# Kernel tuning notes

Measured on AMD Instinct MI355X. Metric: run time of the kernel, lower is better.

Reference implementation:

```python
import jax, jax.numpy as jnp
import numpy as np

B, S, D = 2, 2048, 2048
H = 16
HD = D // H  # 128
THETA = 10000.0


def setup_inputs() -> dict:
    key = jax.random.key(0)
    ks = jax.random.split(key, 5)
    return {
        "hidden_states": jax.random.normal(ks[0], (B, S, D), dtype=jnp.float32),
        "Wq": jax.random.normal(ks[1], (D, D), dtype=jnp.float32) * 0.02,
        "Wk": jax.random.normal(ks[2], (D, D), dtype=jnp.float32) * 0.02,
        "Wv": jax.random.normal(ks[3], (D, D), dtype=jnp.float32) * 0.02,
        "Wo": jax.random.normal(ks[4], (D, D), dtype=jnp.float32) * 0.02,
    }


def _rotate_half(x):
    x1, x2 = x[..., : HD // 2], x[..., HD // 2:]
    return jnp.concatenate([-x2, x1], axis=-1)


def _rope_cos_sin(seq_len, dtype):
    # freqs = 1/theta^(2i/d), i in [0, d/2)
    inv_freq = 1.0 / (THETA ** (jnp.arange(0, HD, 2, dtype=jnp.float32) / HD))
    ang = jnp.arange(seq_len, dtype=jnp.float32)[:, None] * inv_freq[None, :]  # [S, HD/2]
    cos = jnp.cos(ang).astype(dtype)
    sin = jnp.sin(ang).astype(dtype)
    # torch code does cos.repeat(1,1,1,2): tile halves -> [S, HD]
    cos2 = jnp.concatenate([cos, cos], axis=-1)[None, None]  # [1,1,S,HD]
    sin2 = jnp.concatenate([sin, sin], axis=-1)[None, None]
    return cos2, sin2


def reference(hidden_states, Wq, Wk, Wv, Wo):
    b, s, d = hidden_states.shape
    scale = 1.0 / np.sqrt(HD)
    # torch Linear: y = x @ W.T
    def proj(W):
        y = jnp.einsum("bsd,ed->bse", hidden_states, W)
        return y.reshape(b, s, H, HD).transpose(0, 2, 1, 3)  # [b,h,s,hd]
    q, k, v = proj(Wq), proj(Wk), proj(Wv)

    cos, sin = _rope_cos_sin(s, q.dtype)
    q = q * cos + _rotate_half(q) * sin
    k = k * cos + _rotate_half(k) * sin

    scores = jnp.einsum("bhqd,bhkd->bhqk", q, k) * scale
    # causal mask: -inf strictly above diagonal (kv_len == seq_len here)
    causal = jnp.triu(jnp.full((s, s), -jnp.inf, dtype=scores.dtype), k=1)
    scores = scores + causal[None, None]

    attn = jax.nn.softmax(scores.astype(jnp.float32), axis=-1).astype(q.dtype)
    ctx = jnp.einsum("bhqk,bhkd->bhqd", attn, v)
    ctx = ctx.transpose(0, 2, 1, 3).reshape(b, s, d)
    return jnp.einsum("bsd,ed->bse", ctx, Wo)
```

## Files before the change

### kernel.cpp

```cpp
#include <hip/hip_runtime.h>

typedef unsigned short ushort_t;
typedef __bf16 bf16x8 __attribute__((ext_vector_type(8)));
typedef float f32x4 __attribute__((ext_vector_type(4)));

#define S_LEN 2048
#define DMODEL 2048
#define NH 16
#define HDIM 128
#define BATCH 2
#define M_ROWS (BATCH * S_LEN)

__device__ __forceinline__ ushort_t f2bf(float f) {
    union { float f; unsigned u; } v; v.f = f;
    unsigned r = (v.u + 0x7fffu + ((v.u >> 16) & 1u)) >> 16;
    return (ushort_t)r;
}
__device__ __forceinline__ float bf2f(ushort_t u) {
    union { unsigned u; float f; } v; v.u = ((unsigned)u) << 16;
    return v.f;
}

__device__ __forceinline__ void async16(const void* g, void* l) {
    __builtin_amdgcn_global_load_lds(
        (const __attribute__((address_space(1))) void*)g,
        (__attribute__((address_space(3))) void*)l, 16, 0, 0);
}

__global__ void cvt_bf16(const float* __restrict__ in, ushort_t* __restrict__ out, int n4) {
    int i = blockIdx.x * blockDim.x + threadIdx.x;
    if (i >= n4) return;
    float4 f = ((const float4*)in)[i];
    ushort4 u;
    u.x = f2bf(f.x); u.y = f2bf(f.y); u.z = f2bf(f.z); u.w = f2bf(f.w);
    ((ushort4*)out)[i] = u;
}

__global__ void rope_tables(float* __restrict__ cosT, float* __restrict__ sinT) {
    int i = blockIdx.x * blockDim.x + threadIdx.x;
    int s = i >> 6, f = i & 63;
    float inv = powf(10000.0f, -(float)(2 * f) / 128.0f);
    float ang = (float)s * inv;
    cosT[i] = cosf(ang);
    sinT[i] = sinf(ang);
}

__global__ void rope_inplace(ushort_t* __restrict__ Q, ushort_t* __restrict__ K,
                             const float* __restrict__ cosT, const float* __restrict__ sinT) {
    long i = (long)blockIdx.x * blockDim.x + threadIdx.x;
    int f = (int)(i & 63);
    long t = i >> 6;
    int s = (int)(t & (S_LEN - 1));
    int bh = (int)(t >> 11);
    long base = ((long)bh * S_LEN + s) * HDIM;
    float c = cosT[s * 64 + f], sn = sinT[s * 64 + f];
    float a0 = bf2f(Q[base + f]), a1 = bf2f(Q[base + 64 + f]);
    Q[base + f]      = f2bf(a0 * c - a1 * sn);
    Q[base + 64 + f] = f2bf(a1 * c + a0 * sn);
    float b0 = bf2f(K[base + f]), b1 = bf2f(K[base + 64 + f]);
    K[base + f]      = f2bf(b0 * c - b1 * sn);
    K[base + 64 + f] = f2bf(b1 * c + b0 * sn);
}

template <int EPI>
__global__ __launch_bounds__(512) void gemm8(
    const ushort_t* __restrict__ A, const ushort_t* __restrict__ Bm,
    void* __restrict__ C0, void* __restrict__ C1, void* __restrict__ C2,
    int NB, int K) {
    __shared__ __align__(16) ushort_t As[2][128 * 64];
    __shared__ __align__(16) ushort_t Bs[2][256 * 64];
    const int tid = threadIdx.x;
    const int lane = tid & 63;
    const int w = tid >> 6;
    const int wm = w >> 2, wn = w & 3;
    const int fr = lane & 15, g = lane >> 4;
    const int nwg = gridDim.x;
    const int work = (blockIdx.x & 7) * (nwg >> 3) + (blockIdx.x >> 3);
    const int brow = (work / NB) * 128;
    const int bcol = (work % NB) * 256;

    int aRow[2], aK[2], bRow[4], bK[4];
#pragma unroll
    for (int q = 0; q < 2; q++) {
        int d = (q * 512 + tid) * 16;
        int s = d ^ (((d >> 9) & 1) << 5);
        aRow[q] = s >> 7; aK[q] = (s & 127) >> 1;
    }
#pragma unroll
    for (int q = 0; q < 4; q++) {
        int d = (q * 512 + tid) * 16;
        int s = d ^ (((d >> 9) & 1) << 5);
        bRow[q] = s >> 7; bK[q] = (s & 127) >> 1;
    }

    f32x4 acc[4][4];
#pragma unroll
    for (int m = 0; m < 4; m++)
#pragma unroll
        for (int n = 0; n < 4; n++) acc[m][n] = (f32x4){0.f, 0.f, 0.f, 0.f};

    auto stage = [&](int buf, int k0) {
#pragma unroll
        for (int q = 0; q < 2; q++)
            async16(&A[(long)(brow + aRow[q]) * K + k0 + aK[q]], &As[buf][(q * 512 + tid) * 8]);
#pragma unroll
        for (int q = 0; q < 4; q++)
            async16(&Bm[(long)(bcol + bRow[q]) * K + k0 + bK[q]], &Bs[buf][(q * 512 + tid) * 8]);
    };
    auto rdA = [&](int buf, int m, int ks) -> bf16x8 {
        int row = wm * 64 + m * 16 + fr;
        int off = row * 64 + ((ks * 32 + g * 8) ^ (((row >> 2) & 1) << 4));
        return *(const bf16x8*)&As[buf][off];
    };
    auto rdB = [&](int buf, int n, int ks) -> bf16x8 {
        int row = wn * 64 + n * 16 + fr;
        int off = row * 64 + ((ks * 32 + g * 8) ^ (((row >> 2) & 1) << 4));
        return *(const bf16x8*)&Bs[buf][off];
    };

    stage(0, 0);
    __syncthreads();

    const int NT = K / 64;
    int cur = 0;
    for (int kt = 0; kt < NT; ++kt) {
        if (kt + 1 < NT) stage(cur ^ 1, (kt + 1) * 64);
        bf16x8 a0[2][2], a2[2][2], bn[4][2];
#pragma unroll
        for (int m = 0; m < 2; m++)
#pragma unroll
            for (int ks = 0; ks < 2; ks++) a0[m][ks] = rdA(cur, m, ks);
#pragma unroll
        for (int n = 0; n < 2; n++)
#pragma unroll
            for (int ks = 0; ks < 2; ks++) bn[n][ks] = rdB(cur, n, ks);
        __builtin_amdgcn_s_setprio(1);
#pragma unroll
        for (int m = 0; m < 2; m++)
#pragma unroll
            for (int n = 0; n < 2; n++)
#pragma unroll
                for (int ks = 0; ks < 2; ks++)
                    acc[m][n] = __builtin_amdgcn_mfma_f32_16x16x32_bf16(a0[m][ks], bn[n][ks], acc[m][n], 0, 0, 0);
        __builtin_amdgcn_s_setprio(0);
#pragma unroll
        for (int n = 2; n < 4; n++)
#pragma unroll
            for (int ks = 0; ks < 2; ks++) bn[n][ks] = rdB(cur, n, ks);
        __builtin_amdgcn_s_setprio(1);
#pragma unroll
        for (int m = 0; m < 2; m++)
#pragma unroll
            for (int n = 2; n < 4; n++)
#pragma unroll
                for (int ks = 0; ks < 2; ks++)
                    acc[m][n] = __builtin_amdgcn_mfma_f32_16x16x32_bf16(a0[m][ks], bn[n][ks], acc[m][n], 0, 0, 0);
        __builtin_amdgcn_s_setprio(0);
#pragma unroll
        for (int m = 0; m < 2; m++)
#pragma unroll
            for (int ks = 0; ks < 2; ks++) a2[m][ks] = rdA(cur, m + 2, ks);
        __builtin_amdgcn_s_setprio(1);
#pragma unroll
        for (int m = 0; m < 2; m++)
#pragma unroll
            for (int n = 2; n < 4; n++)
#pragma unroll
                for (int ks = 0; ks < 2; ks++)
                    acc[m + 2][n] = __builtin_amdgcn_mfma_f32_16x16x32_bf16(a2[m][ks], bn[n][ks], acc[m + 2][n], 0, 0, 0);
        __builtin_amdgcn_s_setprio(0);
        __builtin_amdgcn_s_setprio(1);
#pragma unroll
        for (int m = 0; m < 2; m++)
#pragma unroll
            for (int n = 0; n < 2; n++)
#pragma unroll
                for (int ks = 0; ks < 2; ks++)
                    acc[m + 2][n] = __builtin_amdgcn_mfma_f32_16x16x32_bf16(a2[m][ks], bn[n][ks], acc[m + 2][n], 0, 0, 0);
        __builtin_amdgcn_s_setprio(0);
        __syncthreads();
        cur ^= 1;
    }

    const int rbase = brow + wm * 64;
    if constexpr (EPI == 0) {
        const int proj = bcol >> 11;
        const int cbase = (bcol & 2047) + wn * 64;
        if (proj < 2) {
            ushort_t* dst = (ushort_t*)(proj == 0 ? C0 : C1);
#pragma unroll
            for (int m = 0; m < 4; m++)
#pragma unroll
                for (int n = 0; n < 4; n++) {
                    int c2 = cbase + n * 16 + fr;
                    int h = c2 >> 7, hd = c2 & 127;
#pragma unroll
                    for (int r = 0; r < 4; r++) {
                        int row = rbase + m * 16 + g * 4 + r;
                        int b = row >> 11, s = row & (S_LEN - 1);
                        dst[(((long)(b * NH + h) * S_LEN) + s) * HDIM + hd] = f2bf(acc[m][n][r]);
                    }
                }
        } else {
            ushort_t* dst = (ushort_t*)C2;
#pragma unroll
            for (int m = 0; m < 4; m++) {
                int row0 = rbase + m * 16 + g * 4;
                int b = row0 >> 11, s0 = row0 & (S_LEN - 1);
#pragma unroll
                for (int n = 0; n < 4; n++) {
                    int c2 = cbase + n * 16 + fr;
                    int h = c2 >> 7, hd = c2 & 127;
                    ushort4 u;
                    u.x = f2bf(acc[m][n][0]); u.y = f2bf(acc[m][n][1]);
                    u.z = f2bf(acc[m][n][2]); u.w = f2bf(acc[m][n][3]);
                    *(ushort4*)&dst[(((long)(b * NH + h) * HDIM) + hd) * S_LEN + s0] = u;
                }
            }
        }
    } else {
        float* dst = (float*)C0;
#pragma unroll
        for (int m = 0; m < 4; m++)
#pragma unroll
            for (int n = 0; n < 4; n++) {
                int col = bcol + wn * 64 + n * 16 + fr;
#pragma unroll
                for (int r = 0; r < 4; r++) {
                    int row = rbase + m * 16 + g * 4 + r;
                    dst[(long)row * DMODEL + col] = acc[m][n][r];
                }
            }
    }
}

__global__ __launch_bounds__(256) void attn_fwd_v4(
    const ushort_t* __restrict__ Q, const ushort_t* __restrict__ K,
    const ushort_t* __restrict__ Vt, ushort_t* __restrict__ ctx) {
    __shared__ __align__(16) ushort_t Ks[2][64 * 128];
    __shared__ __align__(16) ushort_t Vs[2][128 * 64];
    __shared__ __align__(16) ushort_t Pls[4][16 * 64];

    const int tid = threadIdx.x;
    const int lane = tid & 63;
    const int w = tid >> 6;
    const int g = lane >> 4;
    const int fr = lane & 15;
    const int fk = g * 8;

    const int bid = blockIdx.x;
    const int xcd = bid & 7;
    const int t6 = bid >> 3;
    const int bh = xcd + 8 * (t6 & 3);
    const int p = t6 >> 2;
    const int qtA = p, qtB = 31 - p;
    const int b = bh >> 4, h = bh & 15;

    const ushort_t* Qb = Q + (long)bh * S_LEN * HDIM;
    const ushort_t* Kb = K + (long)bh * S_LEN * HDIM;
    const ushort_t* Vb = Vt + (long)bh * HDIM * S_LEN;

    int koff[4], voff[4], kdst[4], vdst[4];
#pragma unroll
    for (int r = 0; r < 4; r++) {
        int ci = r * 256 + tid;
        int krow = ci >> 4, kwc = ci & 15;
        koff[r] = krow * HDIM + ((kwc ^ (krow & 7)) * 8);
        kdst[r] = ci * 8;
        int vrow = ci >> 3, vwc = ci & 7;
        voff[r] = vrow * S_LEN + ((vwc ^ (vrow & 7)) * 8);
        vdst[r] = ci * 8;
    }
    auto stage = [&](int buf, int kv0) {
        const ushort_t* Kg = Kb + (long)kv0 * HDIM;
        const ushort_t* Vg = Vb + kv0;
#pragma unroll
        for (int r = 0; r < 4; r++) async16(Kg + koff[r], &Ks[buf][kdst[r]]);
#pragma unroll
        for (int r = 0; r < 4; r++) async16(Vg + voff[r], &Vs[buf][vdst[r]]);
    };

    int qrow0 = qtA * 64 + w * 16;
    bf16x8 qf[4];
    auto loadQ = [&]() {
#pragma unroll
        for (int t = 0; t < 4; t++)
            qf[t] = *(const bf16x8*)&Qb[(long)(qrow0 + fr) * HDIM + t * 32 + fk];
    };
    loadQ();

    f32x4 o[8];
#pragma unroll
    for (int i = 0; i < 8; i++) o[i] = (f32x4){0.f, 0.f, 0.f, 0.f};
    float mrun = -1e30f, lrun = 0.f;

    const float scale = 0.08838834764831845f;
    long obase = ((long)b * S_LEN) * DMODEL + (long)h * HDIM;
    auto flush = [&]() {
        float inv = 1.0f / lrun;
        long rowb = obase + (long)(qrow0 + fr) * DMODEL;
#pragma unroll
        for (int dt = 0; dt < 8; dt++) {
            ushort4 u;
            u.x = f2bf(o[dt][0] * inv); u.y = f2bf(o[dt][1] * inv);
            u.z = f2bf(o[dt][2] * inv); u.w = f2bf(o[dt][3] * inv);
            *(ushort4*)&ctx[rowb + dt * 16 + g * 4] = u;
        }
    };

    const int ntA = qtA + 1;
    const int ntot = 33;

    stage(0, 0);
    __syncthreads();

    int cur = 0;
    for (int u = 0; u < ntot; ++u) {
        if (u + 1 < ntot) {
            int kvn = (u + 1 < ntA) ? (u + 1) : (u + 1 - ntA);
            stage(cur ^ 1, kvn * 64);
        }
        const int kv0 = ((u < ntA) ? u : (u - ntA)) * 64;
        if (u == ntA) {
            flush();
            qrow0 = qtB * 64 + w * 16;
            loadQ();
#pragma unroll
            for (int i = 0; i < 8; i++) o[i] = (f32x4){0.f, 0.f, 0.f, 0.f};
            mrun = -1e30f; lrun = 0.f;
        }
        if (kv0 <= qrow0 + 15) {
            f32x4 sf[4];
#pragma unroll
            for (int c = 0; c < 4; c++) sf[c] = (f32x4){0.f, 0.f, 0.f, 0.f};
            __builtin_amdgcn_s_setprio(1);
#pragma unroll
            for (int c = 0; c < 4; c++) {
                const int krow = c * 16 + fr;
#pragma unroll
                for (int tt = 0; tt < 4; tt++) {
                    bf16x8 kb = *(const bf16x8*)&Ks[cur][krow * 128 + (((tt * 4 + g) ^ (krow & 7)) * 8)];
                    sf[c] = __builtin_amdgcn_mfma_f32_16x16x32_bf16(kb, qf[tt], sf[c], 0, 0, 0);
                }
            }
            __builtin_amdgcn_s_setprio(0);
            if (kv0 + 63 <= qrow0) {
#pragma unroll
                for (int c = 0; c < 4; c++)
#pragma unroll
                    for (int r = 0; r < 4; r++) sf[c][r] *= scale;
            } else {
                const int q = qrow0 + fr;
#pragma unroll
                for (int c = 0; c < 4; c++)
#pragma unroll
                    for (int r = 0; r < 4; r++) {
                        int kv = kv0 + c * 16 + g * 4 + r;
                        sf[c][r] = (kv <= q) ? sf[c][r] * scale : -1e30f;
                    }
            }
            {
                float vmax = -1e30f;
#pragma unroll
                for (int c = 0; c < 4; c++) {
                    float t0 = fmaxf(fmaxf(sf[c][0], sf[c][1]), fmaxf(sf[c][2], sf[c][3]));
                    vmax = fmaxf(vmax, t0);
                }
                vmax = fmaxf(vmax, __shfl_xor(vmax, 16));
                vmax = fmaxf(vmax, __shfl_xor(vmax, 32));
                if (!__all(vmax - mrun <= 8.f)) {
                    float nm = fmaxf(mrun, vmax);
                    float alpha = __expf(mrun - nm);
                    mrun = nm;
                    lrun *= alpha;
#pragma unroll
                    for (int dt = 0; dt < 8; dt++) o[dt] *= alpha;
                }
                float rs = 0.f;
#pragma unroll
                for (int c = 0; c < 4; c++)
#pragma unroll
                    for (int r = 0; r < 4; r++) {
                        float pv = __expf(sf[c][r] - mrun);
                        sf[c][r] = pv;
                        rs += pv;
                    }
                rs += __shfl_xor(rs, 16);
                rs += __shfl_xor(rs, 32);
                lrun += rs;
            }
#pragma unroll
            for (int c = 0; c < 4; c++) {
                ushort4 u;
                u.x = f2bf(sf[c][0]); u.y = f2bf(sf[c][1]);
                u.z = f2bf(sf[c][2]); u.w = f2bf(sf[c][3]);
                *(ushort4*)&Pls[w][fr * 64 + ((c * 16 + g * 4) ^ ((fr & 7) << 3))] = u;
            }
            bf16x8 pa[2];
#pragma unroll
            for (int hh = 0; hh < 2; hh++)
                pa[hh] = *(const bf16x8*)&Pls[w][fr * 64 + ((hh * 32 + g * 8) ^ ((fr & 7) << 3))];
            __builtin_amdgcn_s_setprio(1);
#pragma unroll
            for (int dt = 0; dt < 8; dt++) {
                const int vrow = dt * 16 + fr;
#pragma unroll
                for (int hh = 0; hh < 2; hh++) {
                    bf16x8 vb = *(const bf16x8*)&Vs[cur][vrow * 64 + (((hh * 4 + g) ^ (vrow & 7)) * 8)];
                    o[dt] = __builtin_amdgcn_mfma_f32_16x16x32_bf16(vb, pa[hh], o[dt], 0, 0, 0);
                }
            }
            __builtin_amdgcn_s_setprio(0);
        }
        __syncthreads();
        cur ^= 1;
    }
    flush();
}

extern "C" void kernel_launch(void* const* d_in, const int* in_sizes, int n_in,
                              void* d_out, int out_size, void* d_ws, size_t ws_size,
                              hipStream_t stream) {
    const float* hs = (const float*)d_in[0];
    const float* Wq = (const float*)d_in[1];
    const float* Wk = (const float*)d_in[2];
    const float* Wv = (const float*)d_in[3];
    const float* Wo = (const float*)d_in[4];
    float* out = (float*)d_out;

    size_t off = 0;
    char* wsb = (char*)d_ws;
    auto carve = [&](size_t bytes) { void* p = wsb + off; off += bytes; return p; };

    ushort_t* Xb   = (ushort_t*)carve((size_t)M_ROWS * DMODEL * 2);
    ushort_t* Wqb  = (ushort_t*)carve((size_t)DMODEL * DMODEL * 2);
    ushort_t* Wkb  = (ushort_t*)carve((size_t)DMODEL * DMODEL * 2);
    ushort_t* Wvb  = (ushort_t*)carve((size_t)DMODEL * DMODEL * 2);
    ushort_t* Wob  = (ushort_t*)carve((size_t)DMODEL * DMODEL * 2);
    ushort_t* Qb   = (ushort_t*)carve((size_t)BATCH * NH * S_LEN * HDIM * 2);
    ushort_t* Kb   = (ushort_t*)carve((size_t)BATCH * NH * S_LEN * HDIM * 2);
    ushort_t* Vtb  = (ushort_t*)carve((size_t)BATCH * NH * S_LEN * HDIM * 2);
    ushort_t* ctxb = (ushort_t*)carve((size_t)M_ROWS * DMODEL * 2);
    float* cosT    = (float*)carve((size_t)S_LEN * 64 * 4);
    float* sinT    = (float*)carve((size_t)S_LEN * 64 * 4);

    const int nX = M_ROWS * DMODEL;
    const int nW = DMODEL * DMODEL;

    cvt_bf16<<<(nX / 4) / 256, 256, 0, stream>>>(hs, Xb, nX / 4);
    cvt_bf16<<<(nW / 4) / 256, 256, 0, stream>>>(Wq, Wqb, nW / 4);
    cvt_bf16<<<(nW / 4) / 256, 256, 0, stream>>>(Wk, Wkb, nW / 4);
    cvt_bf16<<<(nW / 4) / 256, 256, 0, stream>>>(Wv, Wvb, nW / 4);
    cvt_bf16<<<(nW / 4) / 256, 256, 0, stream>>>(Wo, Wob, nW / 4);
    rope_tables<<<(S_LEN * 64) / 256, 256, 0, stream>>>(cosT, sinT);

    gemm8<0><<<(M_ROWS / 128) * (3 * DMODEL / 256), 512, 0, stream>>>(
        Xb, Wqb, Qb, Kb, Vtb, 3 * DMODEL / 256, DMODEL);

    rope_inplace<<<(BATCH * NH * S_LEN * 64) / 256, 256, 0, stream>>>(Qb, Kb, cosT, sinT);

    attn_fwd_v4<<<512, 256, 0, stream>>>(Qb, Kb, Vtb, ctxb);

    gemm8<2><<<(M_ROWS / 128) * (DMODEL / 256), 512, 0, stream>>>(
        ctxb, Wob, out, nullptr, nullptr, DMODEL / 256, DMODEL);
}
```

Measured before the change: 300.9 us.

## Deepen GEMM prefetch with vmcnt waits, XOR swizzle, and XCD column mapping

The GEMM now issues loads two k-tiles ahead, replacing the full __syncthreads with explicit vmcnt waits and raw s_barrier calls. This keeps global-to-LDS copies in flight across iterations and removes a drain per step. The LDS swizzle changes to a per-row 8-way XOR on 16-byte chunks to reduce bank conflicts on fragment reads. Workgroups are also remapped so each XCD owns a contiguous column band, which should improve L2 reuse of B. The hand-written vmcnt(6) assumes exactly six outstanding loads per stage, so it depends on that load count staying fixed.

```diff
diff --git a/kernel.cpp b/kernel.cpp
--- a/kernel.cpp
+++ b/kernel.cpp
@@ -74,23 +74,26 @@
     const int w = tid >> 6;
     const int wm = w >> 2, wn = w & 3;
     const int fr = lane & 15, g = lane >> 4;
-    const int nwg = gridDim.x;
-    const int work = (blockIdx.x & 7) * (nwg >> 3) + (blockIdx.x >> 3);
-    const int brow = (work / NB) * 128;
-    const int bcol = (work % NB) * 256;
+    const int cpx = NB >> 3;
+    const int xcd = blockIdx.x & 7;
+    const int local = blockIdx.x >> 3;
+    const int brow = (local / cpx) * 128;
+    const int bcol = (xcd * cpx + local % cpx) * 256;
 
     int aRow[2], aK[2], bRow[4], bK[4];
 #pragma unroll
     for (int q = 0; q < 2; q++) {
         int d = (q * 512 + tid) * 16;
-        int s = d ^ (((d >> 9) & 1) << 5);
-        aRow[q] = s >> 7; aK[q] = (s & 127) >> 1;
+        int row = d >> 7;
+        int s = d ^ ((row & 7) << 4);
+        aRow[q] = row; aK[q] = (s & 127) >> 1;
     }
 #pragma unroll
     for (int q = 0; q < 4; q++) {
         int d = (q * 512 + tid) * 16;
-        int s = d ^ (((d >> 9) & 1) << 5);
-        bRow[q] = s >> 7; bK[q] = (s & 127) >> 1;
+        int row = d >> 7;
+        int s = d ^ ((row & 7) << 4);
+        bRow[q] = row; bK[q] = (s & 127) >> 1;
     }
 
     f32x4 acc[4][4];
@@ -109,22 +112,30 @@
     };
     auto rdA = [&](int buf, int m, int ks) -> bf16x8 {
         int row = wm * 64 + m * 16 + fr;
-        int off = row * 64 + ((ks * 32 + g * 8) ^ (((row >> 2) & 1) << 4));
-        return *(const bf16x8*)&As[buf][off];
+        int cb = (ks * 64 + g * 16) ^ ((row & 7) << 4);
+        return *(const bf16x8*)((const char*)&As[buf][0] + row * 128 + cb);
     };
     auto rdB = [&](int buf, int n, int ks) -> bf16x8 {
         int row = wn * 64 + n * 16 + fr;
-        int off = row * 64 + ((ks * 32 + g * 8) ^ (((row >> 2) & 1) << 4));
-        return *(const bf16x8*)&Bs[buf][off];
-    };
-
+        int cb = (ks * 64 + g * 16) ^ ((row & 7) << 4);
+        return *(const bf16x8*)((const char*)&Bs[buf][0] + row * 128 + cb);
+    };
+
+    const int NT = K / 64;
     stage(0, 0);
-    __syncthreads();
-
-    const int NT = K / 64;
-    int cur = 0;
+    stage(1, 64);
+
     for (int kt = 0; kt < NT; ++kt) {
-        if (kt + 1 < NT) stage(cur ^ 1, (kt + 1) * 64);
+        const int cur = kt & 1;
+        if (kt + 1 < NT) {
+            asm volatile("s_waitcnt vmcnt(6)" ::: "memory");
+        } else {
+            asm volatile("s_waitcnt vmcnt(0)" ::: "memory");
+        }
+        __builtin_amdgcn_sched_barrier(0);
+        __builtin_amdgcn_s_barrier();
+        __builtin_amdgcn_sched_barrier(0);
+
         bf16x8 a0[2][2], a2[2][2], bn[4][2];
 #pragma unroll
         for (int m = 0; m < 2; m++)
@@ -178,8 +189,10 @@
                 for (int ks = 0; ks < 2; ks++)
                     acc[m + 2][n] = __builtin_amdgcn_mfma_f32_16x16x32_bf16(a2[m][ks], bn[n][ks], acc[m + 2][n], 0, 0, 0);
         __builtin_amdgcn_s_setprio(0);
-        __syncthreads();
-        cur ^= 1;
+
+        __builtin_amdgcn_s_barrier();
+        __builtin_amdgcn_sched_barrier(0);
+        if (kt + 2 < NT) stage(cur, (kt + 2) * 64);
     }
 
     const int rbase = brow + wm * 64;
```

Result: faster. 294.7 us (-2.1%).
